# Kernel tuning notes

Measured on AMD Instinct MI355X. Metric: run time of the kernel, lower is better.

The kernel has to match this reference:

```python
import jax, jax.numpy as jnp
import numpy as np

B, L, K, M, N, P, D = 8, 512, 512, 64, 64, 64, 64  # M == D required for residual add


def _layernorm(x, gamma, beta, eps=1e-3):  # keras LayerNormalization default eps
    mu = jnp.mean(x, axis=-1, keepdims=True)
    var = jnp.var(x, axis=-1, keepdims=True)
    return (x - mu) * jax.lax.rsqrt(var + eps) * gamma + beta


def setup_inputs() -> dict:
    key = jax.random.key(0)
    ks = jax.random.split(key, 5)
    return {
        "q": jax.random.normal(ks[0], (B, L, D), dtype=jnp.float32),
        "k": jax.random.normal(ks[1], (B, K, D), dtype=jnp.float32),
        "vq": jax.random.normal(ks[2], (B, L, M, N), dtype=jnp.float32),
        "vk": jax.random.normal(ks[3], (B, K, P, N), dtype=jnp.float32),
        "vexp": jax.random.normal(ks[4], (B, K, P), dtype=jnp.float32),
        "scale": jnp.ones((), dtype=jnp.float32),      # keras Attention use_scale param (init 1)
        "ln_gamma": jnp.ones((D,), dtype=jnp.float32),  # LayerNormalization gamma
        "ln_beta": jnp.zeros((D,), dtype=jnp.float32),  # LayerNormalization beta
    }


def reference(q, k, vq, vk, vexp, scale, ln_gamma, ln_beta):
    # scores: keras Attention with use_scale -> scale * q @ k^T  (B, L, K)
    scores = scale * jnp.einsum('bld,bkd->blk', q, k)
    # no mask in this call path; plain softmax over keys
    weights = jax.nn.softmax(scores, axis=-1)

    # Original value path (materializes 5D 'blkmp'):
    #   s1 = einsum('blmn,bkpn->blkmp', vq, vk)
    #   v  = einsum('blkmp,bkp->blkm', s1, vexp)
    #   out = einsum('blk,blkm->blm', weights, v)
    # Mathematically identical reassociation that never builds the 5D tensor:
    vkc = jnp.einsum('bkpn,bkp->bkn', vk, vexp)       # contract P first
    tmp = jnp.einsum('blk,bkn->bln', weights, vkc)    # softmax-weighted combine over K
    attn_out = jnp.einsum('blmn,bln->blm', vq, tmp)   # contract N -> (B, L, M)

    # BaseAttentionCell / CrossAttention: residual add + LayerNorm
    return _layernorm(q + attn_out, ln_gamma, ln_beta)
```

## Files before the change

### kernel.cpp

```cpp
#include <hip/hip_runtime.h>


__global__ __launch_bounds__(256) void vkc_kernel(const float* __restrict__ vk,
                                                  const float* __restrict__ vexp,
                                                  float* __restrict__ vkc) {
    const int wave = (blockIdx.x << 2) + (threadIdx.x >> 6);
    const int lane = threadIdx.x & 63;

    const float ve_reg = vexp[wave * 64 + lane];
    const int n0 = (lane & 15) << 2;
    const float* base = vk + (long)wave * 4096;

    float ax = 0.f, ay = 0.f, az = 0.f, aw = 0.f;
    #pragma unroll
    for (int it = 0; it < 16; ++it) {
        const int p = (lane >> 4) + (it << 2);
        const float4 v4 = *(const float4*)(base + p * 64 + n0);
        const float w = __shfl(ve_reg, p, 64);
        ax += v4.x * w; ay += v4.y * w; az += v4.z * w; aw += v4.w * w;
    }
    ax += __shfl_down(ax, 32, 64); ax += __shfl_down(ax, 16, 64);
    ay += __shfl_down(ay, 32, 64); ay += __shfl_down(ay, 16, 64);
    az += __shfl_down(az, 32, 64); az += __shfl_down(az, 16, 64);
    aw += __shfl_down(aw, 32, 64); aw += __shfl_down(aw, 16, 64);

    if ((lane & 48) == 0) {
        float4 r; r.x = ax; r.y = ay; r.z = az; r.w = aw;
        *(float4*)(vkc + wave * 64 + n0) = r;
    }
}

__device__ __forceinline__ void lds_barrier() {
    asm volatile("s_waitcnt lgkmcnt(0)" ::: "memory");
    __builtin_amdgcn_s_barrier();
}

__global__ __launch_bounds__(512) void score_out_kernel(
        const float* __restrict__ q,
        const float* __restrict__ k,
        const float* __restrict__ vkc,
        const float* __restrict__ scale_p,
        const float* __restrict__ vq,
        const float* __restrict__ gamma,
        const float* __restrict__ beta,
        float* __restrict__ out) {
    __shared__ float sc[8][512];
    __shared__ float tp[8][8][64];
    __shared__ float tmp_s[8][64];
    __shared__ float attn_s[8][64];

    const int t = threadIdx.x;
    const int wv = t >> 6;
    const int lane = t & 63;
    const int batch = blockIdx.x >> 6;
    const int l0 = (blockIdx.x & 63) << 3;

    const int row = batch * 512 + l0 + wv;
    const float qv = q[row * 64 + lane];

    const float scale = scale_p[0];
    const float* qbase = q + (batch * 512 + l0) * 64;

    {
        const float4* krow = (const float4*)(k + (batch * 512 + t) * 64);
        float acc[8] = {0.f, 0.f, 0.f, 0.f, 0.f, 0.f, 0.f, 0.f};
        #pragma unroll
        for (int dc = 0; dc < 16; ++dc) {
            const float4 kv = krow[dc];
            #pragma unroll
            for (int l = 0; l < 8; ++l) {
                const float4 qv4 = ((const float4*)(qbase + l * 64))[dc];
                acc[l] += qv4.x * kv.x + qv4.y * kv.y + qv4.z * kv.z + qv4.w * kv.w;
            }
        }
        #pragma unroll
        for (int l = 0; l < 8; ++l) sc[l][t] = scale * acc[l];
    }
    lds_barrier();

    {
        float vv[8]; float mx = -1e30f;
        #pragma unroll
        for (int j = 0; j < 8; ++j) { vv[j] = sc[wv][lane + 64 * j]; mx = fmaxf(mx, vv[j]); }
        #pragma unroll
        for (int off = 32; off; off >>= 1) mx = fmaxf(mx, __shfl_xor(mx, off, 64));
        float s = 0.f;
        #pragma unroll
        for (int j = 0; j < 8; ++j) { vv[j] = __expf(vv[j] - mx); s += vv[j]; }
        #pragma unroll
        for (int off = 32; off; off >>= 1) s += __shfl_xor(s, off, 64);
        const float inv = 1.0f / s;
        #pragma unroll
        for (int j = 0; j < 8; ++j) sc[wv][lane + 64 * j] = vv[j] * inv;
    }
    lds_barrier();

    float4 v[16];
    const float* vql = vq + (long)row * 4096;
    {
        const float* vkcb = vkc + batch * 512 * 64;
        const int ksub = lane >> 4;
        const int n0 = (lane & 15) << 2;
        const int kbeg = wv << 6;
        float4 a[8];
        #pragma unroll
        for (int l = 0; l < 8; ++l) { a[l].x = 0.f; a[l].y = 0.f; a[l].z = 0.f; a[l].w = 0.f; }
        #pragma unroll
        for (int i = 0; i < 16; ++i) {
            v[i] = *(const float4*)(vql + i * 256 + lane * 4);
            const int kk = kbeg + (i << 2) + ksub;
            const float4 v4 = *(const float4*)(vkcb + kk * 64 + n0);
            #pragma unroll
            for (int l = 0; l < 8; ++l) {
                const float w = sc[l][kk];
                a[l].x += w * v4.x; a[l].y += w * v4.y;
                a[l].z += w * v4.z; a[l].w += w * v4.w;
            }
        }
        #pragma unroll
        for (int l = 0; l < 8; ++l) {
            a[l].x += __shfl_down(a[l].x, 32, 64); a[l].x += __shfl_down(a[l].x, 16, 64);
            a[l].y += __shfl_down(a[l].y, 32, 64); a[l].y += __shfl_down(a[l].y, 16, 64);
            a[l].z += __shfl_down(a[l].z, 32, 64); a[l].z += __shfl_down(a[l].z, 16, 64);
            a[l].w += __shfl_down(a[l].w, 32, 64); a[l].w += __shfl_down(a[l].w, 16, 64);
        }
        if (lane < 16) {
            #pragma unroll
            for (int l = 0; l < 8; ++l)
                *(float4*)&tp[wv][l][lane << 2] = a[l];
        }
    }
    lds_barrier();

    {
        float s = tp[0][wv][lane];
        #pragma unroll
        for (int w = 1; w < 8; ++w) s += tp[w][wv][lane];
        tmp_s[wv][lane] = s;
    }

    {
        const int n0 = (lane & 15) << 2;
        const float4 t4 = *(const float4*)&tmp_s[wv][n0];

        #pragma unroll
        for (int it = 0; it < 16; ++it) {
            float part = v[it].x * t4.x + v[it].y * t4.y + v[it].z * t4.z + v[it].w * t4.w;
            part += __shfl_down(part, 8, 16);
            part += __shfl_down(part, 4, 16);
            part += __shfl_down(part, 2, 16);
            part += __shfl_down(part, 1, 16);
            if ((lane & 15) == 0) attn_s[wv][it * 4 + (lane >> 4)] = part;
        }

        const float x = qv + attn_s[wv][lane];
        float s1 = x, s2 = x * x;
        #pragma unroll
        for (int off = 32; off; off >>= 1) {
            s1 += __shfl_xor(s1, off, 64);
            s2 += __shfl_xor(s2, off, 64);
        }
        const float mean = s1 * (1.0f / 64.0f);
        const float var = s2 * (1.0f / 64.0f) - mean * mean;
        const float r = rsqrtf(var + 1e-3f);
        out[row * 64 + lane] = (x - mean) * r * gamma[lane] + beta[lane];
    }
}

extern "C" void kernel_launch(void* const* d_in, const int* in_sizes, int n_in,
                              void* d_out, int out_size, void* d_ws, size_t ws_size,
                              hipStream_t stream) {
    const float* q     = (const float*)d_in[0];
    const float* k     = (const float*)d_in[1];
    const float* vq    = (const float*)d_in[2];
    const float* vk    = (const float*)d_in[3];
    const float* vexp  = (const float*)d_in[4];
    const float* scale = (const float*)d_in[5];
    const float* gamma = (const float*)d_in[6];
    const float* beta  = (const float*)d_in[7];
    float* out = (float*)d_out;

    float* vkc = (float*)d_ws;

    vkc_kernel<<<1024, 256, 0, stream>>>(vk, vexp, vkc);
    score_out_kernel<<<512, 512, 0, stream>>>(q, k, vkc, scale, vq, gamma, beta, out);
}
```

Baseline: 175.0 us.

## Halve rows per block and split vq row across two wave halves

Each block now handles 4 query rows instead of 8, and the launch doubles to 1024 blocks. The vq load and N-contraction for each row are split across two waves, each covering half of the M dimension. This cuts per-thread registers (v[8], a[4]) and spreads the dominant vq stream over more blocks for better occupancy and memory parallelism. In exchange, k is reloaded and the score GEMV is redone twice as often per batch, extra barriers are added, and some waves sit idle during softmax and LayerNorm.

```diff
diff --git a/kernel.cpp b/kernel.cpp
--- a/kernel.cpp
+++ b/kernel.cpp
@@ -44,41 +44,40 @@
         const float* __restrict__ gamma,
         const float* __restrict__ beta,
         float* __restrict__ out) {
-    __shared__ float sc[8][512];
-    __shared__ float tp[8][8][64];
-    __shared__ float tmp_s[8][64];
-    __shared__ float attn_s[8][64];
+    __shared__ float sc[4][512];
+    __shared__ float tp[8][4][64];
+    __shared__ float tmp_s[4][64];
+    __shared__ float attn_s[4][64];
 
     const int t = threadIdx.x;
     const int wv = t >> 6;
     const int lane = t & 63;
-    const int batch = blockIdx.x >> 6;
-    const int l0 = (blockIdx.x & 63) << 3;
-
-    const int row = batch * 512 + l0 + wv;
-    const float qv = q[row * 64 + lane];
+    const int batch = blockIdx.x >> 7;
+    const int l0 = (blockIdx.x & 127) << 2;
 
     const float scale = scale_p[0];
     const float* qbase = q + (batch * 512 + l0) * 64;
 
+    const float qres = q[(batch * 512 + l0 + (wv & 3)) * 64 + lane];
+
     {
         const float4* krow = (const float4*)(k + (batch * 512 + t) * 64);
-        float acc[8] = {0.f, 0.f, 0.f, 0.f, 0.f, 0.f, 0.f, 0.f};
+        float acc[4] = {0.f, 0.f, 0.f, 0.f};
         #pragma unroll
         for (int dc = 0; dc < 16; ++dc) {
             const float4 kv = krow[dc];
             #pragma unroll
-            for (int l = 0; l < 8; ++l) {
+            for (int l = 0; l < 4; ++l) {
                 const float4 qv4 = ((const float4*)(qbase + l * 64))[dc];
                 acc[l] += qv4.x * kv.x + qv4.y * kv.y + qv4.z * kv.z + qv4.w * kv.w;
             }
         }
         #pragma unroll
-        for (int l = 0; l < 8; ++l) sc[l][t] = scale * acc[l];
+        for (int l = 0; l < 4; ++l) sc[l][t] = scale * acc[l];
     }
     lds_barrier();
 
-    {
+    if (wv < 4) {
         float vv[8]; float mx = -1e30f;
         #pragma unroll
         for (int j = 0; j < 8; ++j) { vv[j] = sc[wv][lane + 64 * j]; mx = fmaxf(mx, vv[j]); }
@@ -95,30 +94,32 @@
     }
     lds_barrier();
 
-    float4 v[16];
-    const float* vql = vq + (long)row * 4096;
+    const int row = batch * 512 + l0 + (wv & 3);
+    const int half = wv >> 2;
+    const float* vql = vq + (long)row * 4096 + half * 2048;
+    float4 v[8];
     {
         const float* vkcb = vkc + batch * 512 * 64;
         const int ksub = lane >> 4;
         const int n0 = (lane & 15) << 2;
         const int kbeg = wv << 6;
-        float4 a[8];
+        float4 a[4];
         #pragma unroll
-        for (int l = 0; l < 8; ++l) { a[l].x = 0.f; a[l].y = 0.f; a[l].z = 0.f; a[l].w = 0.f; }
+        for (int l = 0; l < 4; ++l) { a[l].x = 0.f; a[l].y = 0.f; a[l].z = 0.f; a[l].w = 0.f; }
         #pragma unroll
         for (int i = 0; i < 16; ++i) {
-            v[i] = *(const float4*)(vql + i * 256 + lane * 4);
+            if (i < 8) v[i] = *(const float4*)(vql + i * 256 + lane * 4);
             const int kk = kbeg + (i << 2) + ksub;
             const float4 v4 = *(const float4*)(vkcb + kk * 64 + n0);
             #pragma unroll
-            for (int l = 0; l < 8; ++l) {
+            for (int l = 0; l < 4; ++l) {
                 const float w = sc[l][kk];
                 a[l].x += w * v4.x; a[l].y += w * v4.y;
                 a[l].z += w * v4.z; a[l].w += w * v4.w;
             }
         }
         #pragma unroll
-        for (int l = 0; l < 8; ++l) {
+        for (int l = 0; l < 4; ++l) {
             a[l].x += __shfl_down(a[l].x, 32, 64); a[l].x += __shfl_down(a[l].x, 16, 64);
             a[l].y += __shfl_down(a[l].y, 32, 64); a[l].y += __shfl_down(a[l].y, 16, 64);
             a[l].z += __shfl_down(a[l].z, 32, 64); a[l].z += __shfl_down(a[l].z, 16, 64);
@@ -126,34 +127,41 @@
         }
         if (lane < 16) {
             #pragma unroll
-            for (int l = 0; l < 8; ++l)
+            for (int l = 0; l < 4; ++l)
                 *(float4*)&tp[wv][l][lane << 2] = a[l];
         }
     }
     lds_barrier();
 
-    {
-        float s = tp[0][wv][lane];
+    if (t < 256) {
+        const int l = t >> 6, n = t & 63;
+        float s = tp[0][l][n];
         #pragma unroll
-        for (int w = 1; w < 8; ++w) s += tp[w][wv][lane];
-        tmp_s[wv][lane] = s;
+        for (int w = 1; w < 8; ++w) s += tp[w][l][n];
+        tmp_s[l][n] = s;
     }
+    lds_barrier();
 
     {
         const int n0 = (lane & 15) << 2;
-        const float4 t4 = *(const float4*)&tmp_s[wv][n0];
+        const float4 t4 = *(const float4*)&tmp_s[wv & 3][n0];
 
         #pragma unroll
-        for (int it = 0; it < 16; ++it) {
-            float part = v[it].x * t4.x + v[it].y * t4.y + v[it].z * t4.z + v[it].w * t4.w;
+        for (int j = 0; j < 8; ++j) {
+            float part = v[j].x * t4.x + v[j].y * t4.y + v[j].z * t4.z + v[j].w * t4.w;
             part += __shfl_down(part, 8, 16);
             part += __shfl_down(part, 4, 16);
             part += __shfl_down(part, 2, 16);
             part += __shfl_down(part, 1, 16);
-            if ((lane & 15) == 0) attn_s[wv][it * 4 + (lane >> 4)] = part;
+            if ((lane & 15) == 0)
+                attn_s[wv & 3][half * 32 + j * 4 + (lane >> 4)] = part;
         }
+    }
+    lds_barrier();
 
-        const float x = qv + attn_s[wv][lane];
+    if (t < 256) {
+        const int orow = batch * 512 + l0 + wv;
+        const float x = qres + attn_s[wv][lane];
         float s1 = x, s2 = x * x;
         #pragma unroll
         for (int off = 32; off; off >>= 1) {
@@ -163,7 +171,7 @@
         const float mean = s1 * (1.0f / 64.0f);
         const float var = s2 * (1.0f / 64.0f) - mean * mean;
         const float r = rsqrtf(var + 1e-3f);
-        out[row * 64 + lane] = (x - mean) * r * gamma[lane] + beta[lane];
+        out[orow * 64 + lane] = (x - mean) * r * gamma[lane] + beta[lane];
     }
 }
 
@@ -183,5 +191,5 @@
     float* vkc = (float*)d_ws;
 
     vkc_kernel<<<1024, 256, 0, stream>>>(vk, vexp, vkc);
-    score_out_kernel<<<512, 512, 0, stream>>>(q, k, vkc, scale, vq, gamma, beta, out);
+    score_out_kernel<<<1024, 512, 0, stream>>>(q, k, vkc, scale, vq, gamma, beta, out);
 }
```

Result: no change. 176.7 us (+1.0%).
